# Performance work log

Measured on AMD Instinct MI355X. Metric: run time of the kernel, lower is better.

The kernel has to match this reference:

```python
import jax, jax.numpy as jnp
import numpy as np

B, D, H = 64, 1024, 1024  # batch, input_dim, hidden_dim


def setup_inputs() -> dict:
    key = jax.random.key(0)
    k_x, k_inW, k_hW = jax.random.split(key, 3)
    # Observed binary inputs in {0,1} -> Bernoulli-sample branch never taken.
    x = jax.random.randint(k_x, (B, D), 0, 2).astype(jnp.float32)
    # Kaiming-normal init: std = sqrt(2 / fan_in)
    in_W = jax.random.normal(k_inW, (H, D), dtype=jnp.float32) * np.float32(np.sqrt(2.0 / D))
    in_b = jnp.zeros((H,), dtype=jnp.float32)
    h_W = jax.random.normal(k_hW, (D, H), dtype=jnp.float32) * np.float32(np.sqrt(2.0 / H))
    h_b = jnp.zeros((D,), dtype=jnp.float32)
    return {"x": x, "in_W": in_W, "in_b": in_b, "h_W": h_W, "h_b": h_b}


def reference(x, in_W, in_b, h_W, h_b):
    # NADE recurrence: a_i = in_b + sum_{j<i} x_j * in_W[:, j]
    # Vectorized via exclusive cumulative sum of rank-1 contributions.
    contrib = jnp.einsum("bd,hd->bdh", x, in_W)          # [B, D, H]
    cum = jnp.cumsum(contrib, axis=1)
    a = jnp.concatenate([jnp.zeros_like(cum[:, :1]), cum[:, :-1]], axis=1) + in_b  # exclusive
    h = jax.nn.relu(a)                                    # [B, D, H]
    # p_i = sigmoid(relu(a_i) . h_W[i] + h_b[i])
    p_hat = jax.nn.sigmoid(jnp.einsum("bdh,dh->bd", h, h_W) + h_b)  # [B, D]
    return p_hat
```

## Files before the change

kernel.cpp:

```cpp
#include <hip/hip_runtime.h>
#include <hip/hip_bf16.h>

#define B 64
#define D 1024
#define H 1024
#define C 32
#define L (D / C)
#define BG 4
#define NBG (B / BG)
#define HQ 4
#define HP (H / HQ)

__device__ __forceinline__ float dpp_xor1(float v) {
    int i = __builtin_bit_cast(int, v);
    i = __builtin_amdgcn_mov_dpp(i, 0xB1, 0xF, 0xF, true);
    return __builtin_bit_cast(float, i);
}
__device__ __forceinline__ float dpp_xor2(float v) {
    int i = __builtin_bit_cast(int, v);
    i = __builtin_amdgcn_mov_dpp(i, 0x4E, 0xF, 0xF, true);
    return __builtin_bit_cast(float, i);
}

__global__ void __launch_bounds__(256)
k_chunk_sums(const float* __restrict__ x,
             const float* __restrict__ in_W,
             float* __restrict__ S) {
    int blk = blockIdx.x;
    int bg  = blk >> 7;
    int chq = blk & 127;
    int c   = chq >> 2;
    int hq  = chq & 3;
    int b0  = bg * BG;
    int tid = threadIdx.x;
    int h   = hq * HP + tid;

    __shared__ float4 xs4[L];
    if (tid < L) {
        int i = c * L + tid;
        xs4[tid] = make_float4(x[(size_t)b0 * D + i],
                               x[(size_t)(b0 + 1) * D + i],
                               x[(size_t)(b0 + 2) * D + i],
                               x[(size_t)(b0 + 3) * D + i]);
    }

    const float* wrow = &in_W[(size_t)h * D + c * L];
    float wr[L];
    #pragma unroll
    for (int q = 0; q < L / 4; ++q)
        *reinterpret_cast<float4*>(&wr[q * 4]) =
            *reinterpret_cast<const float4*>(wrow + q * 4);

    __syncthreads();

    float acc0 = 0.f, acc1 = 0.f, acc2 = 0.f, acc3 = 0.f;
    #pragma unroll
    for (int j = 0; j < L; ++j) {
        float4 xf = xs4[j];
        float w = wr[j];
        acc0 = fmaf(xf.x, w, acc0);
        acc1 = fmaf(xf.y, w, acc1);
        acc2 = fmaf(xf.z, w, acc2);
        acc3 = fmaf(xf.w, w, acc3);
    }
    S[((size_t)b0 * C + c) * H + h]       = acc0;
    S[((size_t)(b0 + 1) * C + c) * H + h] = acc1;
    S[((size_t)(b0 + 2) * C + c) * H + h] = acc2;
    S[((size_t)(b0 + 3) * C + c) * H + h] = acc3;
}

__global__ void __launch_bounds__(256, 2)
k_nade_main(const float* __restrict__ x,
            const float* __restrict__ in_W,
            const float* __restrict__ in_b,
            const float* __restrict__ h_W,
            const float* __restrict__ S,
            float* __restrict__ Q) {
    int blk = blockIdx.x;
    int bg  = blk >> 7;
    int chq = blk & 127;
    int c   = chq >> 2;
    int hq  = chq & 3;
    int b0  = bg * BG;
    int tid = threadIdx.x;
    int h   = hq * HP + tid;
    int lane = tid & 63;
    int wv = tid >> 6;
    int ph = lane & 3;

    __shared__ float4 xs4[L];
    if (tid < L) {
        int i = c * L + tid;
        xs4[tid] = make_float4(x[(size_t)b0 * D + i],
                               x[(size_t)(b0 + 1) * D + i],
                               x[(size_t)(b0 + 2) * D + i],
                               x[(size_t)(b0 + 3) * D + i]);
    }

    const float* wrow = &in_W[(size_t)h * D + c * L];
    float wr[L];
    #pragma unroll
    for (int q = 0; q < L / 4; ++q)
        *reinterpret_cast<float4*>(&wr[q * 4]) =
            *reinterpret_cast<const float4*>(wrow + q * 4);

    float ib = in_b[h];
    float a0 = ib, a1 = ib, a2 = ib, a3 = ib;
    for (int cc = 0; cc < c; ++cc) {
        a0 += S[((size_t)b0 * C + cc) * H + h];
        a1 += S[((size_t)(b0 + 1) * C + cc) * H + h];
        a2 += S[((size_t)(b0 + 2) * C + cc) * H + h];
        a3 += S[((size_t)(b0 + 3) * C + cc) * H + h];
    }

    __syncthreads();

    bool k0 = (ph == 0), k1 = (ph == 1), k2 = (ph == 2), k3 = (ph == 3);

    float pr0[8], pr1[8], pr2[8], pr3[8];
    #pragma unroll
    for (int s = 0; s < 8; ++s) { pr0[s] = 0.f; pr1[s] = 0.f; pr2[s] = 0.f; pr3[s] = 0.f; }

    #pragma unroll
    for (int il = 0; il < L; ++il) {
        int i = c * L + il;
        float w  = h_W[(size_t)i * H + h];
        float wt = wr[il];
        float4 xf = xs4[il];
        int s = il >> 2;
        bool keep = (il & 3) == 0 ? k0 : ((il & 3) == 1 ? k1 : ((il & 3) == 2 ? k2 : k3));

        float p0 = fmaxf(a0, 0.f) * w;
        float t0 = p0 + dpp_xor1(p0); t0 = t0 + dpp_xor2(t0);
        pr0[s] = keep ? t0 : pr0[s];
        a0 = fmaf(xf.x, wt, a0);

        float p1 = fmaxf(a1, 0.f) * w;
        float t1 = p1 + dpp_xor1(p1); t1 = t1 + dpp_xor2(t1);
        pr1[s] = keep ? t1 : pr1[s];
        a1 = fmaf(xf.y, wt, a1);

        float p2 = fmaxf(a2, 0.f) * w;
        float t2 = p2 + dpp_xor1(p2); t2 = t2 + dpp_xor2(t2);
        pr2[s] = keep ? t2 : pr2[s];
        a2 = fmaf(xf.z, wt, a2);

        float p3 = fmaxf(a3, 0.f) * w;
        float t3 = p3 + dpp_xor1(p3); t3 = t3 + dpp_xor2(t3);
        pr3[s] = keep ? t3 : pr3[s];
        a3 = fmaf(xf.w, wt, a3);
    }

    #pragma unroll
    for (int s = 0; s < 8; ++s) {
        float v;
        v = pr0[s];
        v += __shfl_xor(v, 4, 64); v += __shfl_xor(v, 8, 64);
        v += __shfl_xor(v, 16, 64); v += __shfl_xor(v, 32, 64);
        pr0[s] = v;
        v = pr1[s];
        v += __shfl_xor(v, 4, 64); v += __shfl_xor(v, 8, 64);
        v += __shfl_xor(v, 16, 64); v += __shfl_xor(v, 32, 64);
        pr1[s] = v;
        v = pr2[s];
        v += __shfl_xor(v, 4, 64); v += __shfl_xor(v, 8, 64);
        v += __shfl_xor(v, 16, 64); v += __shfl_xor(v, 32, 64);
        pr2[s] = v;
        v = pr3[s];
        v += __shfl_xor(v, 4, 64); v += __shfl_xor(v, 8, 64);
        v += __shfl_xor(v, 16, 64); v += __shfl_xor(v, 32, 64);
        pr3[s] = v;
    }

    __shared__ float red[4][BG][L];
    if (lane < 4) {
        #pragma unroll
        for (int s = 0; s < 8; ++s) {
            red[wv][0][s * 4 + lane] = pr0[s];
            red[wv][1][s * 4 + lane] = pr1[s];
            red[wv][2][s * 4 + lane] = pr2[s];
            red[wv][3][s * 4 + lane] = pr3[s];
        }
    }
    __syncthreads();

    if (tid < BG * L) {
        int b = tid >> 5;
        int il = tid & 31;
        float t = red[0][b][il] + red[1][b][il] + red[2][b][il] + red[3][b][il];
        Q[((size_t)hq * B + (b0 + b)) * D + c * L + il] = t;
    }
}

__global__ void __launch_bounds__(256)
k_combine(const float* __restrict__ Q,
          const float* __restrict__ h_b,
          float* __restrict__ out) {
    int idx = blockIdx.x * blockDim.x + threadIdx.x;
    if (idx >= B * D) return;
    int d = idx & (D - 1);
    float t = Q[idx] + Q[(size_t)B * D + idx] + Q[2 * (size_t)B * D + idx]
            + Q[3 * (size_t)B * D + idx] + h_b[d];
    out[idx] = 1.0f / (1.0f + expf(-t));
}

extern "C" void kernel_launch(void* const* d_in, const int* in_sizes, int n_in,
                              void* d_out, int out_size, void* d_ws, size_t ws_size,
                              hipStream_t stream) {
    const float* x    = (const float*)d_in[0];
    const float* in_W = (const float*)d_in[1];
    const float* in_b = (const float*)d_in[2];
    const float* h_W  = (const float*)d_in[3];
    const float* h_b  = (const float*)d_in[4];
    float* out = (float*)d_out;

    float* S = (float*)d_ws;
    float* Q = S + (size_t)B * C * H;

    k_chunk_sums<<<NBG * C * HQ, 256, 0, stream>>>(x, in_W, S);

    k_nade_main<<<NBG * C * HQ, 256, 0, stream>>>(x, in_W, in_b, h_W, S, Q);

    k_combine<<<(B * D + 255) / 256, 256, 0, stream>>>(Q, h_b, out);
}
```

Baseline: 48.62 us.

## Stage in_W tiles through LDS with coalesced loads and reverse chunk order

Replaces the per-thread strided float4 row loads of in_W, where each thread reads its own row, with a cooperative load in which each warp reads 32 contiguous columns across rows. The tile is written transposed into padded shared memory, in both kernels. This makes the global loads coalesced and lowers register pressure, at the cost of about 33 KB of LDS per block. The main kernel also reverses chunk order so the blocks with long prefix-sum loops are scheduled first, unrolls that prefix loop, and drops the min-blocks launch bound.

Result: faster. 44.24 us (-9.0%).

```diff
diff --git a/kernel.cpp b/kernel.cpp
--- a/kernel.cpp
+++ b/kernel.cpp
@@ -7,6 +7,8 @@
 #define C 32
 #define L (D / C)
 #define BG 4
+#define NBG (B / NBG_DUMMY)
+#undef NBG
 #define NBG (B / BG)
 #define HQ 4
 #define HP (H / HQ)
@@ -20,6 +22,19 @@
     int i = __builtin_bit_cast(int, v);
     i = __builtin_amdgcn_mov_dpp(i, 0x4E, 0xF, 0xF, true);
     return __builtin_bit_cast(float, i);
+}
+
+__device__ __forceinline__ void load_wt_tile(const float* __restrict__ in_W,
+                                             int hq, int c, int tid,
+                                             float (*wt)[HP + 2]) {
+    const float* base = in_W + (size_t)(hq * HP) * D + c * L;
+    int col = tid & 31;
+    int rg  = tid >> 5;
+    #pragma unroll
+    for (int r = 0; r < 32; ++r) {
+        int row = r * 8 + rg;
+        wt[col][row] = base[(size_t)row * D + col];
+    }
 }
 
 __global__ void __launch_bounds__(256)
@@ -35,7 +50,9 @@
     int tid = threadIdx.x;
     int h   = hq * HP + tid;
 
+    __shared__ float wt[L][HP + 2];
     __shared__ float4 xs4[L];
+
     if (tid < L) {
         int i = c * L + tid;
         xs4[tid] = make_float4(x[(size_t)b0 * D + i],
@@ -43,21 +60,14 @@
                                x[(size_t)(b0 + 2) * D + i],
                                x[(size_t)(b0 + 3) * D + i]);
     }
-
-    const float* wrow = &in_W[(size_t)h * D + c * L];
-    float wr[L];
-    #pragma unroll
-    for (int q = 0; q < L / 4; ++q)
-        *reinterpret_cast<float4*>(&wr[q * 4]) =
-            *reinterpret_cast<const float4*>(wrow + q * 4);
-
+    load_wt_tile(in_W, hq, c, tid, wt);
     __syncthreads();
 
     float acc0 = 0.f, acc1 = 0.f, acc2 = 0.f, acc3 = 0.f;
     #pragma unroll
     for (int j = 0; j < L; ++j) {
+        float w = wt[j][tid];
         float4 xf = xs4[j];
-        float w = wr[j];
         acc0 = fmaf(xf.x, w, acc0);
         acc1 = fmaf(xf.y, w, acc1);
         acc2 = fmaf(xf.z, w, acc2);
@@ -69,7 +79,7 @@
     S[((size_t)(b0 + 3) * C + c) * H + h] = acc3;
 }
 
-__global__ void __launch_bounds__(256, 2)
+__global__ void __launch_bounds__(256)
 k_nade_main(const float* __restrict__ x,
             const float* __restrict__ in_W,
             const float* __restrict__ in_b,
@@ -79,7 +89,7 @@
     int blk = blockIdx.x;
     int bg  = blk >> 7;
     int chq = blk & 127;
-    int c   = chq >> 2;
+    int c   = (C - 1) - (chq >> 2);
     int hq  = chq & 3;
     int b0  = bg * BG;
     int tid = threadIdx.x;
@@ -88,7 +98,10 @@
     int wv = tid >> 6;
     int ph = lane & 3;
 
+    __shared__ float wt[L][HP + 2];
     __shared__ float4 xs4[L];
+    __shared__ float red[4][BG][L];
+
     if (tid < L) {
         int i = c * L + tid;
         xs4[tid] = make_float4(x[(size_t)b0 * D + i],
@@ -96,16 +109,11 @@
                                x[(size_t)(b0 + 2) * D + i],
                                x[(size_t)(b0 + 3) * D + i]);
     }
-
-    const float* wrow = &in_W[(size_t)h * D + c * L];
-    float wr[L];
-    #pragma unroll
-    for (int q = 0; q < L / 4; ++q)
-        *reinterpret_cast<float4*>(&wr[q * 4]) =
-            *reinterpret_cast<const float4*>(wrow + q * 4);
+    load_wt_tile(in_W, hq, c, tid, wt);
 
     float ib = in_b[h];
     float a0 = ib, a1 = ib, a2 = ib, a3 = ib;
+    #pragma unroll 4
     for (int cc = 0; cc < c; ++cc) {
         a0 += S[((size_t)b0 * C + cc) * H + h];
         a1 += S[((size_t)(b0 + 1) * C + cc) * H + h];
@@ -125,7 +133,7 @@
     for (int il = 0; il < L; ++il) {
         int i = c * L + il;
         float w  = h_W[(size_t)i * H + h];
-        float wt = wr[il];
+        float wtv = wt[il][tid];
         float4 xf = xs4[il];
         int s = il >> 2;
         bool keep = (il & 3) == 0 ? k0 : ((il & 3) == 1 ? k1 : ((il & 3) == 2 ? k2 : k3));
@@ -133,22 +141,22 @@
         float p0 = fmaxf(a0, 0.f) * w;
         float t0 = p0 + dpp_xor1(p0); t0 = t0 + dpp_xor2(t0);
         pr0[s] = keep ? t0 : pr0[s];
-        a0 = fmaf(xf.x, wt, a0);
+        a0 = fmaf(xf.x, wtv, a0);
 
         float p1 = fmaxf(a1, 0.f) * w;
         float t1 = p1 + dpp_xor1(p1); t1 = t1 + dpp_xor2(t1);
         pr1[s] = keep ? t1 : pr1[s];
-        a1 = fmaf(xf.y, wt, a1);
+        a1 = fmaf(xf.y, wtv, a1);
 
         float p2 = fmaxf(a2, 0.f) * w;
         float t2 = p2 + dpp_xor1(p2); t2 = t2 + dpp_xor2(t2);
         pr2[s] = keep ? t2 : pr2[s];
-        a2 = fmaf(xf.z, wt, a2);
+        a2 = fmaf(xf.z, wtv, a2);
 
         float p3 = fmaxf(a3, 0.f) * w;
         float t3 = p3 + dpp_xor1(p3); t3 = t3 + dpp_xor2(t3);
         pr3[s] = keep ? t3 : pr3[s];
-        a3 = fmaf(xf.w, wt, a3);
+        a3 = fmaf(xf.w, wtv, a3);
     }
 
     #pragma unroll
@@ -172,7 +180,6 @@
         pr3[s] = v;
     }
 
-    __shared__ float red[4][BG][L];
     if (lane < 4) {
         #pragma unroll
         for (int s = 0; s < 8; ++s) {
```
